# Performance work log

Hardware: AMD Instinct MI355X
Metric: run time of the kernel (lower is better)

## Reference

```python
import jax, jax.numpy as jnp
import numpy as np

K = 16          # neighbors used for attention (knn uses K+1 incl. self)
LRELU = 0.01    # torch LeakyReLU default negative_slope


def setup_inputs() -> dict:
    key = jax.random.key(0)
    ks = jax.random.split(key, 12)
    B, N = 4, 8192
    w = lambda k, shape: (jax.random.normal(k, shape, jnp.float32) * 0.05)
    inp = {
        "x": jax.random.normal(ks[0], (B, N, 3), jnp.float32),
        "global_feat": jax.random.normal(ks[1], (B, 1024), jnp.float32),  # unused by forward (matches source)
        # convs1 = MLP_CONV(3, [64,128]): Conv1d(3,64)+ReLU, Conv1d(64,128)
        "W1": w(ks[2], (64, 3)),    "b1": jnp.zeros((64,), jnp.float32),
        "W2": w(ks[3], (128, 64)),  "b2": jnp.zeros((128,), jnp.float32),
        # convs2: Conv2d(9,64,1x1)+LReLU, Conv2d(64,64,1x1)+LReLU, Conv2d(64,128,1x1)
        "Wc1": w(ks[4], (64, 9)),   "bc1": jnp.zeros((64,), jnp.float32),
        "Wc2": w(ks[5], (64, 64)),  "bc2": jnp.zeros((64,), jnp.float32),
        "Wc3": w(ks[6], (128, 64)), "bc3": jnp.zeros((128,), jnp.float32),
        # conv_query / conv_key: Conv2d(256,256,1x1)
        "Wq": w(ks[7], (256, 256)), "bq": jnp.zeros((256,), jnp.float32),
        "Wk": w(ks[8], (256, 256)), "bk": jnp.zeros((256,), jnp.float32),
    }
    return inp


def _lrelu(t):
    return jnp.where(t >= 0, t, LRELU * t)


def _forward(x, W1, b1, W2, b2, Wc1, bc1, Wc2, bc2, Wc3, bc3, Wq, bq, Wk, bk):
    # convs1: pointwise MLP on coords -> per-point features f [B,N,128]
    f = jax.nn.relu(jnp.einsum('bnc,oc->bno', x, W1) + b1)
    f = jnp.einsum('bnc,oc->bno', f, W2) + b2

    # knn_points(x, x, K=17): squared-distance matrix, nearest-first (self at slot 0)
    sq = jnp.sum(x * x, axis=-1)                              # [B,N]
    d2 = sq[:, :, None] + sq[:, None, :] - 2.0 * jnp.einsum('bnc,bmc->bnm', x, x)
    _, idx = jax.lax.top_k(-d2, K + 1)                        # [B,N,K+1]

    gather = jax.vmap(lambda a, i: a[i])                      # per-batch fancy gather
    knn_x = gather(x, idx)                                    # [B,N,K+1,3]
    knn_f = gather(f, idx)                                    # [B,N,K+1,128]

    rep = jnp.broadcast_to(x[:, :, None, :], knn_x.shape)     # repeat_x
    r = jnp.concatenate([rep, knn_x, rep - knn_x], axis=-1)   # [B,N,K+1,9]
    r = _lrelu(jnp.einsum('bnkc,oc->bnko', r, Wc1) + bc1)
    r = _lrelu(jnp.einsum('bnkc,oc->bnko', r, Wc2) + bc2)
    r = jnp.einsum('bnkc,oc->bnko', r, Wc3) + bc3             # [B,N,K+1,128]

    feat = jnp.concatenate([knn_f, r], axis=-1)               # [B,N,K+1,256]
    q = jnp.einsum('bnkc,oc->bnko', feat[:, :, :1, :], Wq) + bq   # [B,N,1,256]
    k = jnp.einsum('bnkc,oc->bnko', feat[:, :, 1:, :], Wk) + bk   # [B,N,K,256]
    w = jax.nn.softmax(jnp.sum(q * k, axis=-1), axis=-1)      # [B,N,K]
    new_x = jnp.sum(w[..., None] * knn_x[:, :, 1:, :], axis=2)    # [B,N,3]
    return new_x


def reference(x, global_feat, W1, b1, W2, b2, Wc1, bc1, Wc2, bc2, Wc3, bc3, Wq, bq, Wk, bk):
    del global_feat  # present in the torch signature but unused in forward
    return _forward(x, W1, b1, W2, b2, Wc1, bc1, Wc2, bc2, Wc3, bc3, Wq, bq, Wk, bk)
```

## Files before the change

### kernel.cpp

```cpp
#include <hip/hip_runtime.h>
#include <hip/hip_bf16.h>

#define NPTS 8192
#define NB   4

typedef unsigned short u16;
typedef unsigned int   u32;
typedef short bf16x8 __attribute__((ext_vector_type(8)));
typedef float f32x4  __attribute__((ext_vector_type(4)));

static __device__ __forceinline__ float bflo(u32 u){ return __uint_as_float(u << 16); }
static __device__ __forceinline__ float bfhi(u32 u){ return __uint_as_float(u & 0xffff0000u); }
static __device__ __forceinline__ u16 f2bf(float f){
  u32 x = __float_as_uint(f);
  return (u16)((x + 0x7fffu + ((x >> 16) & 1u)) >> 16);
}
static __device__ __forceinline__ float lrelu(float v){ return v >= 0.f ? v : 0.01f * v; }

__global__ __launch_bounds__(256) void k0_prep(const float* __restrict__ Wq, const float* __restrict__ bq,
                                               const float* __restrict__ Wk, const float* __restrict__ Wc3,
                                               u16* __restrict__ Mb, float* __restrict__ u,
                                               u16* __restrict__ Wc3T){
  int oc = blockIdx.x, c = threadIdx.x;
  float acc = 0.f;
  for (int r = 0; r < 256; ++r) acc = fmaf(Wk[r*256 + oc], Wq[r*256 + c], acc);
  Mb[oc*256 + c] = f2bf(acc);
  __shared__ float red[256];
  red[c] = Wk[c*256 + oc] * bq[c];
  __syncthreads();
  for (int s = 128; s > 0; s >>= 1){ if (c < s) red[c] += red[c + s]; __syncthreads(); }
  if (c == 0) u[oc] = red[0];
  if (oc < 32){ int e = oc*256 + c; int h = e >> 7, o = e & 127; Wc3T[h*128 + o] = f2bf(Wc3[o*64 + h]); }
}

__global__ __launch_bounds__(128) void k1_feat(const float* __restrict__ x, const float* __restrict__ W1,
                                               const float* __restrict__ b1, const float* __restrict__ W2,
                                               const float* __restrict__ b2, u16* __restrict__ f){
  __shared__ float xs[16][4];
  __shared__ float hids[16][68];
  __shared__ float W2s[128][68];
  int b = blockIdx.y; int n0 = blockIdx.x * 16; int t = threadIdx.x;
  const float* xb = x + ((size_t)b*NPTS + n0)*3;
  if (t < 48){ int p = t/3, c = t - p*3; xs[p][c] = xb[p*3 + c]; }
  for (int e = t; e < 8192; e += 128) W2s[e >> 6][e & 63] = W2[e];
  __syncthreads();
  {
    int e = t;
    #pragma unroll
    for (int ii = 0; ii < 8; ++ii, e += 128){
      int p = e >> 6, h = e & 63;
      float v = b1[h];
      v = fmaf(W1[h*3+0], xs[p][0], v);
      v = fmaf(W1[h*3+1], xs[p][1], v);
      v = fmaf(W1[h*3+2], xs[p][2], v);
      hids[p][h] = v > 0.f ? v : 0.f;
    }
  }
  __syncthreads();
  int p = t >> 3, og = t & 7;
  float acc[16];
  #pragma unroll
  for (int i = 0; i < 16; ++i) acc[i] = b2[og + 8*i];
  #pragma unroll 4
  for (int c4 = 0; c4 < 16; ++c4){
    float4 hv = *(const float4*)&hids[p][c4*4];
    #pragma unroll
    for (int i = 0; i < 16; ++i){
      float4 wv = *(const float4*)&W2s[og + 8*i][c4*4];
      acc[i] = fmaf(wv.x, hv.x, acc[i]); acc[i] = fmaf(wv.y, hv.y, acc[i]);
      acc[i] = fmaf(wv.z, hv.z, acc[i]); acc[i] = fmaf(wv.w, hv.w, acc[i]);
    }
  }
  u16* fb = f + ((size_t)b*NPTS + n0)*128;
  #pragma unroll
  for (int i = 0; i < 16; ++i) fb[p*128 + og + 8*i] = f2bf(acc[i]);
}

#define K2_FLUSH8() do { \
    _Pragma("unroll") \
    for (int s = 0; s < 8; ++s){ \
      int2 pr = *(const int2*)(bufp + s*4096); \
      float d = (s < cnt) ? __int_as_float(pr.x) : __builtin_inff(); \
      int ii = pr.y; \
      bool pk = bd[16] > d; \
      _Pragma("unroll") \
      for (int k = 16; k >= 1; --k){ \
        bool pk1 = bd[k-1] > d; \
        float nd = pk1 ? bd[k-1] : d; \
        int   ni = pk1 ? bi[k-1] : ii; \
        if (pk){ bd[k] = nd; bi[k] = ni; } \
        pk = pk1; \
      } \
      if (pk){ bd[0] = d; bi[0] = ii; } \
    } \
    cnt = 0; } while (0)

__global__ __launch_bounds__(512) void k2_knn(const float* __restrict__ x, int* __restrict__ idxout){
#pragma clang fp contract(off)
  __shared__ __align__(16) char smem[69632];
  int t = threadIdx.x, lane = t & 63, w = t >> 6;
  int b = blockIdx.y;
  const float* xb = x + (size_t)b*NPTS*3;
  int q = blockIdx.x*64 + lane;
  float qx = xb[q*3+0], qy = xb[q*3+1], qz = xb[q*3+2];
  float qsq = (qx*qx + qy*qy) + qz*qz;
  float bd[17]; int bi[17];
  #pragma unroll
  for (int k = 0; k < 17; ++k){ bd[k] = __builtin_inff(); bi[k] = 0; }
  float4* tile = (float4*)smem;
  float*  tauv = (float*)(smem + 8192);
  char*   bufp = smem + 10240 + t*8;
  tauv[t] = __builtin_inff();
  __syncthreads();
  int cnt = 0;
  float gate = __builtin_inff();
  int c0 = w * 1024;
  for (int t0 = 0; t0 < 1024; t0 += 64){
    int m = c0 + t0 + lane;
    float cx = xb[m*3+0], cy = xb[m*3+1], cz = xb[m*3+2];
    float csq = (cx*cx + cy*cy) + cz*cz;
    tile[w*64 + lane] = make_float4(cx, cy, cz, csq);
    for (int j = 0; j < 64; ++j){
      float4 cd = tile[w*64 + j];
      float dt = (qx*cd.x + qy*cd.y) + qz*cd.z;
      float d2 = (qsq + cd.w) - 2.0f*dt;
      bool push = d2 < gate;
      if (__any(push)){
        if (push){
          *(int2*)(bufp + cnt*4096) = make_int2(__float_as_int(d2), c0 + t0 + j);
          ++cnt;
        }
        if (__any(cnt >= 8)){
          K2_FLUSH8();
          gate = fminf(gate, bd[16]);
        }
      }
    }
    tauv[t] = bd[16];
    float tm = fminf(tauv[lane], tauv[64 + lane]);
    tm = fminf(tm, fminf(tauv[128 + lane], tauv[192 + lane]));
    tm = fminf(tm, fminf(tauv[256 + lane], tauv[320 + lane]));
    tm = fminf(tm, fminf(tauv[384 + lane], tauv[448 + lane]));
    gate = fminf(tm, bd[16]);
  }
  K2_FLUSH8();
  __syncthreads();
  float* md = (float*)smem;
  int*   mi = (int*)(smem + 34816);
  {
    int base = (w*64 + lane)*17;
    #pragma unroll
    for (int k = 0; k < 17; ++k){ md[base + k] = bd[k]; mi[base + k] = bi[k]; }
  }
  __syncthreads();
  if (w == 0){
    int p0=0,p1=0,p2=0,p3=0,p4=0,p5=0,p6=0,p7=0;
    int* op = idxout + ((size_t)b*NPTS + q)*17;
    int base = lane*17;
    for (int k = 0; k < 17; ++k){
      float h0 = md[        base + p0];
      float h1 = md[1088  + base + p1];
      float h2 = md[2176  + base + p2];
      float h3 = md[3264  + base + p3];
      float h4 = md[4352  + base + p4];
      float h5 = md[5440  + base + p5];
      float h6 = md[6528  + base + p6];
      float h7 = md[7616  + base + p7];
      float best = h0; int ws = 0;
      if (h1 < best){ best = h1; ws = 1; }
      if (h2 < best){ best = h2; ws = 2; }
      if (h3 < best){ best = h3; ws = 3; }
      if (h4 < best){ best = h4; ws = 4; }
      if (h5 < best){ best = h5; ws = 5; }
      if (h6 < best){ best = h6; ws = 6; }
      if (h7 < best){ best = h7; ws = 7; }
      int pp = (ws==0)?p0:(ws==1)?p1:(ws==2)?p2:(ws==3)?p3:(ws==4)?p4:(ws==5)?p5:(ws==6)?p6:p7;
      op[k] = mi[ws*1088 + base + pp];
      p0 += (ws==0); p1 += (ws==1); p2 += (ws==2); p3 += (ws==3);
      p4 += (ws==4); p5 += (ws==5); p6 += (ws==6); p7 += (ws==7);
    }
  }
}

__global__ __launch_bounds__(256) void k3_qt(const float* __restrict__ x, const int* __restrict__ idx,
    const u16* __restrict__ f, const u16* __restrict__ Mb, const float* __restrict__ u,
    const u16* __restrict__ Wc3T,
    const float* __restrict__ Wc1, const float* __restrict__ bc1,
    const float* __restrict__ Wc2, const float* __restrict__ bc2,
    const float* __restrict__ bc3, float* __restrict__ qg){
  __shared__ __align__(16) char smem[73088];
  u16*   featb = (u16*)smem;
  float* qtBs  = (float*)(smem + 16896);
  float* h1s   = (float*)(smem + 16896);
  float* h2s   = (float*)(smem + 25600);
  float* Wc1s  = (float*)(smem + 34304);
  float* Wc2s  = (float*)(smem + 36608);
  u16*   W3sD  = (u16*)(smem + 36608);
  u16*   W3s   = (u16*)(smem + 54016);
  float* bcs   = (float*)(smem + 71424);
  float* xns   = (float*)(smem + 71936);
  float* xgs   = (float*)(smem + 72448);
  int*   idx0s = (int*)(smem + 72960);

  int b = blockIdx.y; int n0 = blockIdx.x * 32; int t = threadIdx.x;
  const int p3 = t >> 3, hg = t & 7;

  if (t < 32) idx0s[t] = idx[((size_t)b*NPTS + n0 + t)*17];
  {
    const float* xb = x + ((size_t)b*NPTS + n0)*3;
    if (t < 96){ int p = t/3, c = t - p*3; xns[p*4 + c] = xb[p*3 + c]; }
  }
  if (t < 128) bcs[t] = (t < 64) ? bc1[t] : bc2[t - 64];
  for (int e = t; e < 576; e += 256) Wc1s[e] = Wc1[e];
  for (int e = t; e < 4096; e += 256) Wc2s[(e >> 6)*68 + (e & 63)] = Wc2[e];
  __syncthreads();
  if (t < 96){ int p = t/3, c = t - p*3; xgs[p*4 + c] = x[((size_t)b*NPTS + idx0s[p])*3 + c]; }
  {
    int cg = t & 7;
    const uint4* fsrc = (const uint4*)(f + ((size_t)b*NPTS + idx0s[p3])*128) + cg*2;
    uint4 A = fsrc[0], B = fsrc[1];
    uint4* dst = (uint4*)&featb[p3*264 + cg*16];
    dst[0] = A; dst[1] = B;
  }
  __syncthreads();
  {
    float rv0 = xns[p3*4+0], rv1 = xns[p3*4+1], rv2 = xns[p3*4+2];
    float rv3 = xgs[p3*4+0], rv4 = xgs[p3*4+1], rv5 = xgs[p3*4+2];
    float rv6 = rv0 - rv3, rv7 = rv1 - rv4, rv8 = rv2 - rv5;
    #pragma unroll
    for (int i = 0; i < 8; ++i){
      int h = hg + 8*i;
      const float* wr = &Wc1s[h*9];
      float v = bcs[h];
      v = fmaf(wr[0], rv0, v); v = fmaf(wr[1], rv1, v); v = fmaf(wr[2], rv2, v);
      v = fmaf(wr[3], rv3, v); v = fmaf(wr[4], rv4, v); v = fmaf(wr[5], rv5, v);
      v = fmaf(wr[6], rv6, v); v = fmaf(wr[7], rv7, v); v = fmaf(wr[8], rv8, v);
      h1s[p3*68 + h] = lrelu(v);
    }
  }
  __syncthreads();
  {
    #pragma unroll
    for (int i = 0; i < 8; ++i){
      int h = hg + 8*i;
      float v = bcs[64 + h];
      const float* wr = &Wc2s[h*68];
      const float* ar = &h1s[p3*68];
      #pragma unroll
      for (int c4 = 0; c4 < 16; ++c4){
        float4 wv = *(const float4*)(wr + c4*4);
        float4 av = *(const float4*)(ar + c4*4);
        v = fmaf(wv.x, av.x, v); v = fmaf(wv.y, av.y, v);
        v = fmaf(wv.z, av.z, v); v = fmaf(wv.w, av.w, v);
      }
      h2s[p3*68 + h] = lrelu(v);
    }
  }
  __syncthreads();
  for (int e = t; e < 4096; e += 256) *(u32*)&W3s[(e >> 6)*136 + (e & 63)*2] = ((const u32*)Wc3T)[e];
  __syncthreads();
  {
    int og = hg;
    float4 a0 = *(const float4*)&bc3[og*16 + 0];
    float4 a1 = *(const float4*)&bc3[og*16 + 4];
    float4 a2 = *(const float4*)&bc3[og*16 + 8];
    float4 a3 = *(const float4*)&bc3[og*16 + 12];
    for (int h = 0; h < 64; ++h){
      float hv = h2s[p3*68 + h];
      const u32* wp = (const u32*)&W3s[h*136 + og*16];
      uint4 A = *(const uint4*)wp; uint4 B = *(const uint4*)(wp + 4);
      a0.x = fmaf(bflo(A.x), hv, a0.x); a0.y = fmaf(bfhi(A.x), hv, a0.y);
      a0.z = fmaf(bflo(A.y), hv, a0.z); a0.w = fmaf(bfhi(A.y), hv, a0.w);
      a1.x = fmaf(bflo(A.z), hv, a1.x); a1.y = fmaf(bfhi(A.z), hv, a1.y);
      a1.z = fmaf(bflo(A.w), hv, a1.z); a1.w = fmaf(bfhi(A.w), hv, a1.w);
      a2.x = fmaf(bflo(B.x), hv, a2.x); a2.y = fmaf(bfhi(B.x), hv, a2.y);
      a2.z = fmaf(bflo(B.y), hv, a2.z); a2.w = fmaf(bfhi(B.y), hv, a2.w);
      a3.x = fmaf(bflo(B.z), hv, a3.x); a3.y = fmaf(bfhi(B.z), hv, a3.y);
      a3.z = fmaf(bflo(B.w), hv, a3.z); a3.w = fmaf(bfhi(B.w), hv, a3.w);
    }
    u16* dst = &featb[p3*264 + 128 + og*16];
    u32 pw[8];
    pw[0] = (u32)f2bf(a0.x) | ((u32)f2bf(a0.y) << 16);
    pw[1] = (u32)f2bf(a0.z) | ((u32)f2bf(a0.w) << 16);
    pw[2] = (u32)f2bf(a1.x) | ((u32)f2bf(a1.y) << 16);
    pw[3] = (u32)f2bf(a1.z) | ((u32)f2bf(a1.w) << 16);
    pw[4] = (u32)f2bf(a2.x) | ((u32)f2bf(a2.y) << 16);
    pw[5] = (u32)f2bf(a2.z) | ((u32)f2bf(a2.w) << 16);
    pw[6] = (u32)f2bf(a3.x) | ((u32)f2bf(a3.y) << 16);
    pw[7] = (u32)f2bf(a3.z) | ((u32)f2bf(a3.w) << 16);
    ((uint4*)dst)[0] = make_uint4(pw[0], pw[1], pw[2], pw[3]);
    ((uint4*)dst)[1] = make_uint4(pw[4], pw[5], pw[6], pw[7]);
  }
  __syncthreads();
  {
    int lane = t & 63, wv = t >> 6;
    int l15 = lane & 15, kq = lane >> 4;
    f32x4 acc[2][4];
    #pragma unroll
    for (int rt = 0; rt < 2; ++rt)
      #pragma unroll
      for (int ct = 0; ct < 4; ++ct)
        acc[rt][ct] = (f32x4){0.f, 0.f, 0.f, 0.f};
    #pragma unroll
    for (int ks = 0; ks < 8; ++ks){
      bf16x8 a0 = *(const bf16x8*)&featb[l15*264 + ks*32 + kq*8];
      bf16x8 a1 = *(const bf16x8*)&featb[(16 + l15)*264 + ks*32 + kq*8];
      #pragma unroll
      for (int ct = 0; ct < 4; ++ct){
        int oc = wv*64 + ct*16 + l15;
        bf16x8 bb = *(const bf16x8*)(Mb + oc*256 + ks*32 + kq*8);
        acc[0][ct] = __builtin_amdgcn_mfma_f32_16x16x32_bf16(a0, bb, acc[0][ct], 0, 0, 0);
        acc[1][ct] = __builtin_amdgcn_mfma_f32_16x16x32_bf16(a1, bb, acc[1][ct], 0, 0, 0);
      }
    }
    if (wv < 2){
      float* qgb = qg + ((size_t)b*NPTS + n0)*192;
      #pragma unroll
      for (int ct = 0; ct < 4; ++ct){
        int oc = wv*64 + ct*16 + l15;
        float uv = u[oc];
        #pragma unroll
        for (int rt = 0; rt < 2; ++rt){
          #pragma unroll
          for (int j = 0; j < 4; ++j){
            int p = rt*16 + kq*4 + j;
            qgb[(size_t)p*192 + oc] = acc[rt][ct][j] + uv;
          }
        }
      }
    } else {
      #pragma unroll
      for (int ct = 0; ct < 4; ++ct){
        int oc = (wv - 2)*64 + ct*16 + l15;
        float uv = u[128 + oc];
        #pragma unroll
        for (int rt = 0; rt < 2; ++rt){
          #pragma unroll
          for (int j = 0; j < 4; ++j){
            int p = rt*16 + kq*4 + j;
            qtBs[p*132 + oc] = acc[rt][ct][j] + uv;
          }
        }
      }
    }
  }
  __syncthreads();
  for (int e = t; e < 4096; e += 256) *(u32*)&W3sD[(e >> 6)*136 + (e & 63)*2] = ((const u32*)Wc3T)[e];
  __syncthreads();
  {
    float gacc[8];
    #pragma unroll
    for (int i = 0; i < 8; ++i) gacc[i] = 0.f;
    for (int o8 = 0; o8 < 16; ++o8){
      const float* qr = &qtBs[p3*132 + o8*8];
      float4 qa = *(const float4*)qr; float4 qb4 = *(const float4*)(qr + 4);
      #pragma unroll
      for (int i = 0; i < 8; ++i){
        int h = hg + 8*i;
        const uint4 WU = *(const uint4*)&W3sD[h*136 + o8*8];
        float acc = gacc[i];
        acc = fmaf(bflo(WU.x), qa.x, acc); acc = fmaf(bfhi(WU.x), qa.y, acc);
        acc = fmaf(bflo(WU.y), qa.z, acc); acc = fmaf(bfhi(WU.y), qa.w, acc);
        acc = fmaf(bflo(WU.z), qb4.x, acc); acc = fmaf(bfhi(WU.z), qb4.y, acc);
        acc = fmaf(bflo(WU.w), qb4.z, acc); acc = fmaf(bfhi(WU.w), qb4.w, acc);
        gacc[i] = acc;
      }
    }
    float* qgb = qg + ((size_t)b*NPTS + n0)*192;
    #pragma unroll
    for (int i = 0; i < 8; ++i) qgb[p3*192 + 128 + hg + 8*i] = gacc[i];
  }
}

__global__ __launch_bounds__(256) void k4_attn(const float* __restrict__ x, const int* __restrict__ idx,
    const u16* __restrict__ f, const float* __restrict__ qg,
    const float* __restrict__ Wc1, const float* __restrict__ bc1,
    const float* __restrict__ Wc2, const float* __restrict__ bc2,
    float* __restrict__ out){
  __shared__ int idxs[16][17];
  __shared__ float xns[16][4];
  __shared__ float qgs[16][196];
  __shared__ float Wc1s[576];
  __shared__ float Wc2s[64][68];
  __shared__ float bcs[128];
  int b = blockIdx.y; int n0 = blockIdx.x * 16; int t = threadIdx.x;
  for (int e = t; e < 272; e += 256){ int p = e/17, k = e - p*17; idxs[p][k] = idx[((size_t)b*NPTS + n0 + p)*17 + k]; }
  if (t < 48){ int p = t/3, c = t - p*3; xns[p][c] = x[((size_t)b*NPTS + n0 + p)*3 + c]; }
  if (t < 128) bcs[t] = (t < 64) ? bc1[t] : bc2[t - 64];
  for (int e = t; e < 576; e += 256) Wc1s[e] = Wc1[e];
  for (int e = t; e < 4096; e += 256) Wc2s[e >> 6][e & 63] = Wc2[e];
  {
    const float* src = qg + ((size_t)b*NPTS + n0)*192;
    for (int e = t; e < 3072; e += 256){ int p = e/192, c = e - p*192; qgs[p][c] = src[e]; }
  }
  __syncthreads();
  int p = t >> 4, j = t & 15;
  int nidx = idxs[p][j + 1];
  const float* xr = x + ((size_t)b*NPTS + nidx)*3;
  float cx = xr[0], cy = xr[1], cz = xr[2];
  float rx = xns[p][0], ry = xns[p][1], rz = xns[p][2];
  float dx = rx - cx, dy = ry - cy, dz = rz - cz;
  float logit = 0.f;
  {
    const u32* fr = (const u32*)(f + ((size_t)b*NPTS + nidx)*128);
    #pragma unroll
    for (int c8 = 0; c8 < 16; ++c8){
      uint4 FU = *(const uint4*)(fr + c8*4);
      const float* qr = &qgs[p][c8*8];
      float4 qa = *(const float4*)qr; float4 qb4 = *(const float4*)(qr + 4);
      logit = fmaf(bflo(FU.x), qa.x, logit); logit = fmaf(bfhi(FU.x), qa.y, logit);
      logit = fmaf(bflo(FU.y), qa.z, logit); logit = fmaf(bfhi(FU.y), qa.w, logit);
      logit = fmaf(bflo(FU.z), qb4.x, logit); logit = fmaf(bfhi(FU.z), qb4.y, logit);
      logit = fmaf(bflo(FU.w), qb4.z, logit); logit = fmaf(bfhi(FU.w), qb4.w, logit);
    }
  }
  float h1r[64];
  #pragma unroll
  for (int h = 0; h < 64; ++h){
    const float* wr = &Wc1s[h*9];
    float v = bcs[h];
    v = fmaf(wr[0], rx, v); v = fmaf(wr[1], ry, v); v = fmaf(wr[2], rz, v);
    v = fmaf(wr[3], cx, v); v = fmaf(wr[4], cy, v); v = fmaf(wr[5], cz, v);
    v = fmaf(wr[6], dx, v); v = fmaf(wr[7], dy, v); v = fmaf(wr[8], dz, v);
    h1r[h] = lrelu(v);
  }
  for (int h = 0; h < 64; ++h){
    float v = bcs[64 + h];
    const float* wr = &Wc2s[h][0];
    #pragma unroll
    for (int c4 = 0; c4 < 16; ++c4){
      float4 wv = *(const float4*)(wr + c4*4);
      v = fmaf(wv.x, h1r[c4*4+0], v); v = fmaf(wv.y, h1r[c4*4+1], v);
      v = fmaf(wv.z, h1r[c4*4+2], v); v = fmaf(wv.w, h1r[c4*4+3], v);
    }
    logit = fmaf(qgs[p][128 + h], lrelu(v), logit);
  }
  float mx = logit;
  #pragma unroll
  for (int s = 1; s < 16; s <<= 1) mx = fmaxf(mx, __shfl_xor(mx, s, 16));
  float ev = expf(logit - mx);
  float sum = ev;
  #pragma unroll
  for (int s = 1; s < 16; s <<= 1) sum += __shfl_xor(sum, s, 16);
  float wgt = ev / sum;
  float ox = wgt*cx, oy = wgt*cy, oz = wgt*cz;
  #pragma unroll
  for (int s = 1; s < 16; s <<= 1){
    ox += __shfl_xor(ox, s, 16); oy += __shfl_xor(oy, s, 16); oz += __shfl_xor(oz, s, 16);
  }
  if (j == 0){
    float* op = out + ((size_t)b*NPTS + n0 + p)*3;
    op[0] = ox; op[1] = oy; op[2] = oz;
  }
}

extern "C" void kernel_launch(void* const* d_in, const int* in_sizes, int n_in,
                              void* d_out, int out_size, void* d_ws, size_t ws_size,
                              hipStream_t stream){
  (void)in_sizes; (void)n_in; (void)out_size; (void)ws_size;
  const float* x   = (const float*)d_in[0];
  const float* W1  = (const float*)d_in[2];
  const float* b1  = (const float*)d_in[3];
  const float* W2  = (const float*)d_in[4];
  const float* b2  = (const float*)d_in[5];
  const float* Wc1 = (const float*)d_in[6];
  const float* bc1 = (const float*)d_in[7];
  const float* Wc2 = (const float*)d_in[8];
  const float* bc2 = (const float*)d_in[9];
  const float* Wc3 = (const float*)d_in[10];
  const float* bc3 = (const float*)d_in[11];
  const float* Wq  = (const float*)d_in[12];
  const float* bq  = (const float*)d_in[13];
  const float* Wk  = (const float*)d_in[14];
  float* out = (float*)d_out;

  char* ws = (char*)d_ws;
  u16*   Mb   = (u16*)(ws + 0);
  float* u    = (float*)(ws + 131072);
  u16*   Wc3T = (u16*)(ws + 132096);
  u16*   fbuf = (u16*)(ws + (1u << 20));
  int*   idxb = (int*)(ws + (16u << 20));
  float* qgb  = (float*)(ws + (32u << 20));

  k0_prep<<<dim3(256), dim3(256), 0, stream>>>(Wq, bq, Wk, Wc3, Mb, u, Wc3T);
  k1_feat<<<dim3(512, NB), dim3(128), 0, stream>>>(x, W1, b1, W2, b2, fbuf);
  k2_knn<<<dim3(128, NB), dim3(512), 0, stream>>>(x, idxb);
  k3_qt<<<dim3(256, NB), dim3(256), 0, stream>>>(x, idxb, fbuf, Mb, u, Wc3T, Wc1, bc1, Wc2, bc2, bc3, qgb);
  k4_attn<<<dim3(512, NB), dim3(256), 0, stream>>>(x, idxb, fbuf, qgb, Wc1, bc1, Wc2, bc2, out);
}
```

Measured before the change: 472.6 us.

## Use MFMA for attention Wc2 layer and batch KNN candidate tests by four

In k4_attn, the per-thread scalar 64x64 Wc2 matvec is replaced by bf16 MFMA 16x16x32 tiles. Hidden activations are staged as bf16 in shared memory and Wc2 is pre-converted to bf16 in k0_prep. The softmax and weighted sum are reorganised around the MFMA output layout. Separately, the KNN inner loop now evaluates four candidates before a single wave vote, flushes at a lower buffer threshold, and updates the shared tau early. This cuts FMA and branch overhead at the cost of bf16 rounding in the second conv layer.

```diff
diff --git a/kernel.cpp b/kernel.cpp
--- a/kernel.cpp
+++ b/kernel.cpp
@@ -19,8 +19,9 @@
 
 __global__ __launch_bounds__(256) void k0_prep(const float* __restrict__ Wq, const float* __restrict__ bq,
                                                const float* __restrict__ Wk, const float* __restrict__ Wc3,
+                                               const float* __restrict__ Wc2,
                                                u16* __restrict__ Mb, float* __restrict__ u,
-                                               u16* __restrict__ Wc3T){
+                                               u16* __restrict__ Wc3T, u16* __restrict__ Wc2p){
   int oc = blockIdx.x, c = threadIdx.x;
   float acc = 0.f;
   for (int r = 0; r < 256; ++r) acc = fmaf(Wk[r*256 + oc], Wq[r*256 + c], acc);
@@ -31,6 +32,7 @@
   for (int s = 128; s > 0; s >>= 1){ if (c < s) red[c] += red[c + s]; __syncthreads(); }
   if (c == 0) u[oc] = red[0];
   if (oc < 32){ int e = oc*256 + c; int h = e >> 7, o = e & 127; Wc3T[h*128 + o] = f2bf(Wc3[o*64 + h]); }
+  if (oc >= 32 && oc < 48){ int e = (oc - 32)*256 + c; Wc2p[e] = f2bf(Wc2[e]); }
 }
 
 __global__ __launch_bounds__(128) void k1_feat(const float* __restrict__ x, const float* __restrict__ W1,
@@ -120,19 +122,27 @@
     float cx = xb[m*3+0], cy = xb[m*3+1], cz = xb[m*3+2];
     float csq = (cx*cx + cy*cy) + cz*cz;
     tile[w*64 + lane] = make_float4(cx, cy, cz, csq);
-    for (int j = 0; j < 64; ++j){
-      float4 cd = tile[w*64 + j];
-      float dt = (qx*cd.x + qy*cd.y) + qz*cd.z;
-      float d2 = (qsq + cd.w) - 2.0f*dt;
-      bool push = d2 < gate;
-      if (__any(push)){
-        if (push){
-          *(int2*)(bufp + cnt*4096) = make_int2(__float_as_int(d2), c0 + t0 + j);
-          ++cnt;
+    for (int j0 = 0; j0 < 64; j0 += 4){
+      float d2v[4];
+      #pragma unroll
+      for (int s = 0; s < 4; ++s){
+        float4 cd = tile[w*64 + j0 + s];
+        float dt = (qx*cd.x + qy*cd.y) + qz*cd.z;
+        d2v[s] = (qsq + cd.w) - 2.0f*dt;
+      }
+      float mn = fminf(fminf(d2v[0], d2v[1]), fminf(d2v[2], d2v[3]));
+      if (__any(mn < gate)){
+        #pragma unroll
+        for (int s = 0; s < 4; ++s){
+          if (d2v[s] < gate){
+            *(int2*)(bufp + cnt*4096) = make_int2(__float_as_int(d2v[s]), c0 + t0 + j0 + s);
+            ++cnt;
+          }
         }
-        if (__any(cnt >= 8)){
+        if (__any(cnt >= 5)){
           K2_FLUSH8();
           gate = fminf(gate, bd[16]);
+          tauv[t] = bd[16];
         }
       }
     }
@@ -375,82 +385,149 @@
 __global__ __launch_bounds__(256) void k4_attn(const float* __restrict__ x, const int* __restrict__ idx,
     const u16* __restrict__ f, const float* __restrict__ qg,
     const float* __restrict__ Wc1, const float* __restrict__ bc1,
-    const float* __restrict__ Wc2, const float* __restrict__ bc2,
+    const float* __restrict__ bc2, const u16* __restrict__ Wc2p,
     float* __restrict__ out){
-  __shared__ int idxs[16][17];
+  __shared__ int   idxs[16][17];
   __shared__ float xns[16][4];
   __shared__ float qgs[16][196];
   __shared__ float Wc1s[576];
-  __shared__ float Wc2s[64][68];
   __shared__ float bcs[128];
+  __shared__ float xjs[256][4];
+  __shared__ float flog[256];
+  __shared__ u16   h1t[256][76];
   int b = blockIdx.y; int n0 = blockIdx.x * 16; int t = threadIdx.x;
   for (int e = t; e < 272; e += 256){ int p = e/17, k = e - p*17; idxs[p][k] = idx[((size_t)b*NPTS + n0 + p)*17 + k]; }
   if (t < 48){ int p = t/3, c = t - p*3; xns[p][c] = x[((size_t)b*NPTS + n0 + p)*3 + c]; }
   if (t < 128) bcs[t] = (t < 64) ? bc1[t] : bc2[t - 64];
   for (int e = t; e < 576; e += 256) Wc1s[e] = Wc1[e];
-  for (int e = t; e < 4096; e += 256) Wc2s[e >> 6][e & 63] = Wc2[e];
   {
     const float* src = qg + ((size_t)b*NPTS + n0)*192;
     for (int e = t; e < 3072; e += 256){ int p = e/192, c = e - p*192; qgs[p][c] = src[e]; }
   }
   __syncthreads();
-  int p = t >> 4, j = t & 15;
-  int nidx = idxs[p][j + 1];
-  const float* xr = x + ((size_t)b*NPTS + nidx)*3;
-  float cx = xr[0], cy = xr[1], cz = xr[2];
-  float rx = xns[p][0], ry = xns[p][1], rz = xns[p][2];
-  float dx = rx - cx, dy = ry - cy, dz = rz - cz;
-  float logit = 0.f;
-  {
-    const u32* fr = (const u32*)(f + ((size_t)b*NPTS + nidx)*128);
-    #pragma unroll
-    for (int c8 = 0; c8 < 16; ++c8){
-      uint4 FU = *(const uint4*)(fr + c8*4);
-      const float* qr = &qgs[p][c8*8];
-      float4 qa = *(const float4*)qr; float4 qb4 = *(const float4*)(qr + 4);
-      logit = fmaf(bflo(FU.x), qa.x, logit); logit = fmaf(bfhi(FU.x), qa.y, logit);
-      logit = fmaf(bflo(FU.y), qa.z, logit); logit = fmaf(bfhi(FU.y), qa.w, logit);
-      logit = fmaf(bflo(FU.z), qb4.x, logit); logit = fmaf(bfhi(FU.z), qb4.y, logit);
-      logit = fmaf(bflo(FU.w), qb4.z, logit); logit = fmaf(bfhi(FU.w), qb4.w, logit);
-    }
-  }
-  float h1r[64];
-  #pragma unroll
-  for (int h = 0; h < 64; ++h){
-    const float* wr = &Wc1s[h*9];
-    float v = bcs[h];
-    v = fmaf(wr[0], rx, v); v = fmaf(wr[1], ry, v); v = fmaf(wr[2], rz, v);
-    v = fmaf(wr[3], cx, v); v = fmaf(wr[4], cy, v); v = fmaf(wr[5], cz, v);
-    v = fmaf(wr[6], dx, v); v = fmaf(wr[7], dy, v); v = fmaf(wr[8], dz, v);
-    h1r[h] = lrelu(v);
-  }
-  for (int h = 0; h < 64; ++h){
-    float v = bcs[64 + h];
-    const float* wr = &Wc2s[h][0];
-    #pragma unroll
-    for (int c4 = 0; c4 < 16; ++c4){
-      float4 wv = *(const float4*)(wr + c4*4);
-      v = fmaf(wv.x, h1r[c4*4+0], v); v = fmaf(wv.y, h1r[c4*4+1], v);
-      v = fmaf(wv.z, h1r[c4*4+2], v); v = fmaf(wv.w, h1r[c4*4+3], v);
-    }
-    logit = fmaf(qgs[p][128 + h], lrelu(v), logit);
-  }
-  float mx = logit;
-  #pragma unroll
-  for (int s = 1; s < 16; s <<= 1) mx = fmaxf(mx, __shfl_xor(mx, s, 16));
-  float ev = expf(logit - mx);
-  float sum = ev;
-  #pragma unroll
-  for (int s = 1; s < 16; s <<= 1) sum += __shfl_xor(sum, s, 16);
-  float wgt = ev / sum;
-  float ox = wgt*cx, oy = wgt*cy, oz = wgt*cz;
-  #pragma unroll
-  for (int s = 1; s < 16; s <<= 1){
-    ox += __shfl_xor(ox, s, 16); oy += __shfl_xor(oy, s, 16); oz += __shfl_xor(oz, s, 16);
-  }
-  if (j == 0){
-    float* op = out + ((size_t)b*NPTS + n0 + p)*3;
-    op[0] = ox; op[1] = oy; op[2] = oz;
+  {
+    int p = t >> 4, j = t & 15;
+    int nidx = idxs[p][j + 1];
+    const float* xr = x + ((size_t)b*NPTS + nidx)*3;
+    float cx = xr[0], cy = xr[1], cz = xr[2];
+    *(float4*)&xjs[t][0] = make_float4(cx, cy, cz, 0.f);
+    float rx = xns[p][0], ry = xns[p][1], rz = xns[p][2];
+    float dx = rx - cx, dy = ry - cy, dz = rz - cz;
+    float logit = 0.f;
+    {
+      const u32* fr = (const u32*)(f + ((size_t)b*NPTS + nidx)*128);
+      #pragma unroll
+      for (int c8 = 0; c8 < 16; ++c8){
+        uint4 FU = *(const uint4*)(fr + c8*4);
+        const float* qr = &qgs[p][c8*8];
+        float4 qa = *(const float4*)qr; float4 qb4 = *(const float4*)(qr + 4);
+        logit = fmaf(bflo(FU.x), qa.x, logit); logit = fmaf(bfhi(FU.x), qa.y, logit);
+        logit = fmaf(bflo(FU.y), qa.z, logit); logit = fmaf(bfhi(FU.y), qa.w, logit);
+        logit = fmaf(bflo(FU.z), qb4.x, logit); logit = fmaf(bfhi(FU.z), qb4.y, logit);
+        logit = fmaf(bflo(FU.w), qb4.z, logit); logit = fmaf(bfhi(FU.w), qb4.w, logit);
+      }
+    }
+    flog[t] = logit;
+    float h1r[64];
+    #pragma unroll
+    for (int h = 0; h < 64; ++h){
+      const float* wr = &Wc1s[h*9];
+      float v = bcs[h];
+      v = fmaf(wr[0], rx, v); v = fmaf(wr[1], ry, v); v = fmaf(wr[2], rz, v);
+      v = fmaf(wr[3], cx, v); v = fmaf(wr[4], cy, v); v = fmaf(wr[5], cz, v);
+      v = fmaf(wr[6], dx, v); v = fmaf(wr[7], dy, v); v = fmaf(wr[8], dz, v);
+      h1r[h] = lrelu(v);
+    }
+    u16* hrow = &h1t[t][0];
+    #pragma unroll
+    for (int c8 = 0; c8 < 8; ++c8){
+      u32 w0 = (u32)f2bf(h1r[c8*8+0]) | ((u32)f2bf(h1r[c8*8+1]) << 16);
+      u32 w1 = (u32)f2bf(h1r[c8*8+2]) | ((u32)f2bf(h1r[c8*8+3]) << 16);
+      u32 w2 = (u32)f2bf(h1r[c8*8+4]) | ((u32)f2bf(h1r[c8*8+5]) << 16);
+      u32 w3 = (u32)f2bf(h1r[c8*8+6]) | ((u32)f2bf(h1r[c8*8+7]) << 16);
+      *(uint4*)&hrow[c8*8] = make_uint4(w0, w1, w2, w3);
+    }
+  }
+  __syncthreads();
+  {
+    int lane = t & 63, wv = t >> 6;
+    int l15 = lane & 15, kq = lane >> 4;
+    f32x4 acc[4][4];
+    #pragma unroll
+    for (int rt = 0; rt < 4; ++rt)
+      #pragma unroll
+      for (int ct = 0; ct < 4; ++ct)
+        acc[rt][ct] = (f32x4){0.f, 0.f, 0.f, 0.f};
+    #pragma unroll
+    for (int ks = 0; ks < 2; ++ks){
+      bf16x8 av[4];
+      #pragma unroll
+      for (int rt = 0; rt < 4; ++rt)
+        av[rt] = *(const bf16x8*)&h1t[wv*64 + rt*16 + l15][ks*32 + kq*8];
+      #pragma unroll
+      for (int ct = 0; ct < 4; ++ct){
+        bf16x8 bv = *(const bf16x8*)(Wc2p + (ct*16 + l15)*64 + ks*32 + kq*8);
+        #pragma unroll
+        for (int rt = 0; rt < 4; ++rt)
+          acc[rt][ct] = __builtin_amdgcn_mfma_f32_16x16x32_bf16(av[rt], bv, acc[rt][ct], 0, 0, 0);
+      }
+    }
+    float lg[4][4];
+    #pragma unroll
+    for (int rt = 0; rt < 4; ++rt)
+      #pragma unroll
+      for (int reg = 0; reg < 4; ++reg) lg[rt][reg] = 0.f;
+    #pragma unroll
+    for (int ct = 0; ct < 4; ++ct){
+      int col = ct*16 + l15;
+      float b2v = bcs[64 + col];
+      #pragma unroll
+      for (int rt = 0; rt < 4; ++rt){
+        float gv = qgs[wv*4 + rt][128 + col];
+        #pragma unroll
+        for (int reg = 0; reg < 4; ++reg){
+          float h2 = lrelu(acc[rt][ct][reg] + b2v);
+          lg[rt][reg] = fmaf(gv, h2, lg[rt][reg]);
+        }
+      }
+    }
+    #pragma unroll
+    for (int s = 1; s < 16; s <<= 1){
+      #pragma unroll
+      for (int rt = 0; rt < 4; ++rt)
+        #pragma unroll
+        for (int reg = 0; reg < 4; ++reg)
+          lg[rt][reg] += __shfl_xor(lg[rt][reg], s, 64);
+    }
+    #pragma unroll
+    for (int rt = 0; rt < 4; ++rt){
+      float4 fl = *(const float4*)&flog[(wv*4 + rt)*16 + kq*4];
+      float l0 = lg[rt][0] + fl.x, l1 = lg[rt][1] + fl.y;
+      float l2 = lg[rt][2] + fl.z, l3 = lg[rt][3] + fl.w;
+      float mx = fmaxf(fmaxf(l0, l1), fmaxf(l2, l3));
+      mx = fmaxf(mx, __shfl_xor(mx, 16, 64));
+      mx = fmaxf(mx, __shfl_xor(mx, 32, 64));
+      float e0 = expf(l0 - mx), e1 = expf(l1 - mx), e2 = expf(l2 - mx), e3 = expf(l3 - mx);
+      float sm = (e0 + e1) + (e2 + e3);
+      sm += __shfl_xor(sm, 16, 64);
+      sm += __shfl_xor(sm, 32, 64);
+      int rbase = (wv*4 + rt)*16 + kq*4;
+      float4 x0 = *(const float4*)&xjs[rbase + 0][0];
+      float4 x1 = *(const float4*)&xjs[rbase + 1][0];
+      float4 x2 = *(const float4*)&xjs[rbase + 2][0];
+      float4 x3 = *(const float4*)&xjs[rbase + 3][0];
+      float ox = e0*x0.x + e1*x1.x + e2*x2.x + e3*x3.x;
+      float oy = e0*x0.y + e1*x1.y + e2*x2.y + e3*x3.y;
+      float oz = e0*x0.z + e1*x1.z + e2*x2.z + e3*x3.z;
+      ox += __shfl_xor(ox, 16, 64); ox += __shfl_xor(ox, 32, 64);
+      oy += __shfl_xor(oy, 16, 64); oy += __shfl_xor(oy, 32, 64);
+      oz += __shfl_xor(oz, 16, 64); oz += __shfl_xor(oz, 32, 64);
+      if (kq == 0 && l15 == rt){
+        float inv = 1.f / sm;
+        float* op = out + ((size_t)b*NPTS + n0 + wv*4 + rt)*3;
+        op[0] = ox * inv; op[1] = oy * inv; op[2] = oz * inv;
+      }
+    }
   }
 }
 
@@ -478,13 +555,14 @@
   u16*   Mb   = (u16*)(ws + 0);
   float* u    = (float*)(ws + 131072);
   u16*   Wc3T = (u16*)(ws + 132096);
+  u16*   Wc2p = (u16*)(ws + 153600);
   u16*   fbuf = (u16*)(ws + (1u << 20));
   int*   idxb = (int*)(ws + (16u << 20));
   float* qgb  = (float*)(ws + (32u << 20));
 
-  k0_prep<<<dim3(256), dim3(256), 0, stream>>>(Wq, bq, Wk, Wc3, Mb, u, Wc3T);
+  k0_prep<<<dim3(256), dim3(256), 0, stream>>>(Wq, bq, Wk, Wc3, Wc2, Mb, u, Wc3T, Wc2p);
   k1_feat<<<dim3(512, NB), dim3(128), 0, stream>>>(x, W1, b1, W2, b2, fbuf);
   k2_knn<<<dim3(128, NB), dim3(512), 0, stream>>>(x, idxb);
   k3_qt<<<dim3(256, NB), dim3(256), 0, stream>>>(x, idxb, fbuf, Mb, u, Wc3T, Wc1, bc1, Wc2, bc2, bc3, qgb);
-  k4_attn<<<dim3(512, NB), dim3(256), 0, stream>>>(x, idxb, fbuf, qgb, Wc1, bc1, Wc2, bc2, out);
-}
+  k4_attn<<<dim3(512, NB), dim3(256), 0, stream>>>(x, idxb, fbuf, qgb, Wc1, bc1, bc2, Wc2p, out);
+}
```

Result: faster. 457.1 us (-3.3%).
